# Performance work log

Hardware: AMD Instinct MI355X
Metric: run time of the kernel (lower is better)

## Reference

```python
import jax, jax.numpy as jnp
import numpy as np

B, N, F_IN, F_OUT = 8, 2048, 512, 512


def setup_inputs() -> dict:
    key = jax.random.key(0)
    k1, k2, k3, k4 = jax.random.split(key, 4)
    X = jax.random.normal(k1, (B, N, F_IN), dtype=jnp.float32)
    A = jax.random.uniform(k2, (B, N, N), dtype=jnp.float32)
    # nn.Linear params (kaiming-uniform-ish scale is irrelevant for correctness)
    bound = 1.0 / np.sqrt(F_IN)
    W = jax.random.uniform(k3, (F_IN, F_OUT), dtype=jnp.float32, minval=-bound, maxval=bound)
    b = jax.random.uniform(k4, (F_OUT,), dtype=jnp.float32, minval=-bound, maxval=bound)
    return {"X": X, "A": A, "W": W, "b": b}


def reference(X, A, W, b):
    # A' = A + I  (self-loops)
    A_hat = A + jnp.eye(A.shape[-1], dtype=A.dtype)
    # D^{-1/2}: per-row degree of A'.  torch builds diag_embed + two bmms;
    # mathematically identical to broadcasted row/column scaling.
    d_inv_sqrt = A_hat.sum(axis=-1) ** -0.5                      # [B, N]
    L = A_hat * d_inv_sqrt[:, :, None] * d_inv_sqrt[:, None, :]  # [B, N, N]
    x = X @ W + b                                                # [B, N, F_out]
    return jnp.einsum('bij,bjf->bif', L, x)
```

## Files before the change

### kernel.cpp

```cpp
#include <hip/hip_runtime.h>

#define B_ 8
#define N_ 2048
#define FIN_ 512
#define FOUT_ 512

typedef __attribute__((ext_vector_type(8))) short short8;
typedef __attribute__((ext_vector_type(4))) float floatx4;
typedef __attribute__((ext_vector_type(4))) unsigned short ushortx4;
typedef __attribute__((ext_vector_type(8))) unsigned short ushortx8;

__device__ inline unsigned short f2bf(float f) {
    union { float f; unsigned int u; } x; x.f = f;
    unsigned int r = x.u + 0x7FFFu + ((x.u >> 16) & 1u);
    return (unsigned short)(r >> 16);
}

__device__ inline void glds16(const void* g, void* l) {
    __builtin_amdgcn_global_load_lds(
        (const __attribute__((address_space(1))) void*)g,
        (__attribute__((address_space(3))) void*)l, 16, 0, 0);
}

__global__ __launch_bounds__(256) void degree_cast_kernel(
    const float* __restrict__ A, float* __restrict__ dinv,
    unsigned short* __restrict__ Abf) {
    int row = blockIdx.x;
    size_t base = (size_t)row * N_;
    const float4* A4 = (const float4*)(A + base);
    int t = threadIdx.x;
    float4 v0 = A4[t];
    float4 v1 = A4[t + 256];
    ushortx4 p0, p1;
    p0[0] = f2bf(v0.x); p0[1] = f2bf(v0.y); p0[2] = f2bf(v0.z); p0[3] = f2bf(v0.w);
    p1[0] = f2bf(v1.x); p1[1] = f2bf(v1.y); p1[2] = f2bf(v1.z); p1[3] = f2bf(v1.w);
    *(ushortx4*)(Abf + base + t * 4) = p0;
    *(ushortx4*)(Abf + base + (t + 256) * 4) = p1;
    float s = v0.x + v0.y + v0.z + v0.w + v1.x + v1.y + v1.z + v1.w;
#pragma unroll
    for (int off = 32; off > 0; off >>= 1) s += __shfl_down(s, off, 64);
    __shared__ float red[4];
    if ((t & 63) == 0) red[t >> 6] = s;
    __syncthreads();
    if (t == 0) dinv[row] = rsqrtf(red[0] + red[1] + red[2] + red[3] + 1.0f);
}

__global__ __launch_bounds__(256) void castX_kernel(const float* __restrict__ X,
                                                    unsigned short* __restrict__ Xbf) {
    size_t e0 = ((size_t)blockIdx.x * 256 + threadIdx.x) * 8;
    float4 a0 = *(const float4*)(X + e0);
    float4 a1 = *(const float4*)(X + e0 + 4);
    float av[8] = {a0.x, a0.y, a0.z, a0.w, a1.x, a1.y, a1.z, a1.w};
    ushortx8 p;
#pragma unroll
    for (int r = 0; r < 8; ++r) p[r] = f2bf(av[r]);
    *(ushortx8*)(Xbf + e0) = p;
}

__global__ __launch_bounds__(256) void transposeW_kernel(const float* __restrict__ W,
                                                         unsigned short* __restrict__ Wt) {
    __shared__ float tile[32][33];
    int bx = blockIdx.x * 32;
    int by = blockIdx.y * 32;
    int tx = threadIdx.x, ty = threadIdx.y;
#pragma unroll
    for (int r = 0; r < 32; r += 8)
        tile[ty + r][tx] = W[(size_t)(by + ty + r) * FOUT_ + bx + tx];
    __syncthreads();
#pragma unroll
    for (int r = 0; r < 32; r += 8)
        Wt[(size_t)(bx + ty + r) * FIN_ + by + tx] = f2bf(tile[tx][ty + r]);
}


__global__ __launch_bounds__(256) void gemm1_kernel(
    const unsigned short* __restrict__ Abase,
    const unsigned short* __restrict__ Btbase,
    unsigned short* __restrict__ XwT,
    const float* __restrict__ bias,
    const float* __restrict__ dinv) {
    __shared__ __align__(16) char smem[65536];

    int t = threadIdx.x;
    int lane = t & 63;
    int wave = t >> 6;
    int wr = wave >> 1, wc = wave & 1;
    int q = lane >> 4, m = lane & 15;
    int n0 = blockIdx.x * 128;
    int m0 = blockIdx.y * 128;

    int srow = t >> 3;
    int scol = (((t & 7) ^ (srow & 7)) * 8);
    int x0 = ((q ^ (m & 7)) * 16);
    int x1 = x0 ^ 64;

    floatx4 acc[4][4];
#pragma unroll
    for (int mi = 0; mi < 4; ++mi)
#pragma unroll
        for (int ni = 0; ni < 4; ++ni)
            acc[mi][ni] = (floatx4){0.f, 0.f, 0.f, 0.f};

    const unsigned short* gA = Abase + (size_t)(m0 + srow) * FIN_ + scol;
    const unsigned short* gB = Btbase + (size_t)(n0 + srow) * FIN_ + scol;

#define STAGE1(bufi) do {                                              \
        char* lA = smem + (bufi) * 32768 + wave * 1024;                \
        char* lB = smem + (bufi) * 32768 + 16384 + wave * 1024;        \
        _Pragma("unroll")                                              \
        for (int u = 0; u < 4; ++u) {                                  \
            glds16(gA + (size_t)(u * 32) * FIN_, lA + u * 4096);       \
            glds16(gB + (size_t)(u * 32) * FIN_, lB + u * 4096);       \
        }                                                              \
        gA += 64; gB += 64;                                            \
    } while (0)

    STAGE1(0);
    STAGE1(1);

    const int NT = FIN_ / 64;
    for (int kt = 0; kt < NT; ++kt) {
        if (kt < NT - 1) asm volatile("s_waitcnt vmcnt(8)" ::: "memory");
        else             asm volatile("s_waitcnt vmcnt(0)" ::: "memory");
        __builtin_amdgcn_sched_barrier(0);
        __builtin_amdgcn_s_barrier();
        const char* As = smem + (kt & 1) * 32768;
        const char* Bs = As + 16384;
        short8 af0[4], bf0[4], af1[4], bf1[4];
#pragma unroll
        for (int mi = 0; mi < 4; ++mi)
            af0[mi] = *(const short8*)(As + (wr * 64 + mi * 16 + m) * 128 + x0);
#pragma unroll
        for (int ni = 0; ni < 4; ++ni)
            bf0[ni] = *(const short8*)(Bs + (wc * 64 + ni * 16 + m) * 128 + x0);
#pragma unroll
        for (int mi = 0; mi < 4; ++mi)
            af1[mi] = *(const short8*)(As + (wr * 64 + mi * 16 + m) * 128 + x1);
#pragma unroll
        for (int ni = 0; ni < 4; ++ni)
            bf1[ni] = *(const short8*)(Bs + (wc * 64 + ni * 16 + m) * 128 + x1);
        asm volatile("s_waitcnt lgkmcnt(8)" ::: "memory");
        __builtin_amdgcn_sched_barrier(0);
        __builtin_amdgcn_s_setprio(1);
#pragma unroll
        for (int mi = 0; mi < 4; ++mi)
#pragma unroll
            for (int ni = 0; ni < 4; ++ni)
                acc[mi][ni] = __builtin_amdgcn_mfma_f32_16x16x32_bf16(
                    af0[mi], bf0[ni], acc[mi][ni], 0, 0, 0);
        __builtin_amdgcn_s_setprio(0);
        asm volatile("s_waitcnt lgkmcnt(0)" ::: "memory");
        __builtin_amdgcn_sched_barrier(0);
        __builtin_amdgcn_s_barrier();
        if (kt + 2 < NT) STAGE1(kt & 1);
        __builtin_amdgcn_sched_barrier(0);
        __builtin_amdgcn_s_setprio(1);
#pragma unroll
        for (int mi = 0; mi < 4; ++mi)
#pragma unroll
            for (int ni = 0; ni < 4; ++ni)
                acc[mi][ni] = __builtin_amdgcn_mfma_f32_16x16x32_bf16(
                    af1[mi], bf1[ni], acc[mi][ni], 0, 0, 0);
        __builtin_amdgcn_s_setprio(0);
    }
#undef STAGE1

    unsigned short* T = (unsigned short*)smem;
#pragma unroll
    for (int mi = 0; mi < 4; ++mi) {
        int row = wr * 64 + mi * 16 + q * 4;
        float4 dv = *(const float4*)(dinv + m0 + row);
        float dr[4] = {dv.x, dv.y, dv.z, dv.w};
#pragma unroll
        for (int ni = 0; ni < 4; ++ni) {
            int col = wc * 64 + ni * 16 + m;
            float bv = bias[n0 + col];
            ushortx4 pk;
#pragma unroll
            for (int r = 0; r < 4; ++r) pk[r] = f2bf((acc[mi][ni][r] + bv) * dr[r]);
            *(ushortx4*)(T + col * 136 + row) = pk;
        }
    }
    __syncthreads();
    int f  = t >> 1;
    int c0 = (t & 1) * 64;
    int bb = m0 >> 11;
    int node0 = (m0 & 2047) + c0;
    unsigned short* dst = XwT + ((size_t)bb * FOUT_ + n0 + f) * N_ + node0;
    const unsigned short* src = T + f * 136 + c0;
#pragma unroll
    for (int u = 0; u < 8; ++u)
        *(ushortx8*)(dst + u * 8) = *(const ushortx8*)(src + u * 8);
}

__global__ __launch_bounds__(128) void gemm2_kernel(
    const unsigned short* __restrict__ Abf,
    const unsigned short* __restrict__ XwT,
    const float* __restrict__ dinv,
    float* __restrict__ out) {
    __shared__ __align__(16) char smem[24576];
    char* As = smem;
    char* Bs = smem + 8192;

    int t = threadIdx.x;
    int lane = t & 63;
    int wave = t >> 6;
    int q = lane >> 4, m = lane & 15;

    int id = blockIdx.x;
    int b  = id & 7;
    int s  = id >> 3;
    int n0 = (s & 3) * 128;
    int m0 = (s >> 2) * 64;

    const unsigned short* Ab = Abf + (size_t)b * N_ * N_;
    const unsigned short* Bb = XwT + (size_t)b * FOUT_ * N_;

    int srow = t >> 3;
    int scol = (((t & 7) ^ (srow & 7)) * 8);
    int x0 = ((q ^ (m & 7)) * 16);
    int x1 = x0 ^ 64;

    floatx4 acc[4][4];
#pragma unroll
    for (int mi = 0; mi < 4; ++mi)
#pragma unroll
        for (int ni = 0; ni < 4; ++ni)
            acc[mi][ni] = (floatx4){0.f, 0.f, 0.f, 0.f};

    const unsigned short* gA = Ab + (size_t)(m0 + srow) * N_ + scol;
    const unsigned short* gB = Bb + (size_t)(n0 + srow) * N_ + scol;
    char* lA = As + wave * 1024;
    char* lB = Bs + wave * 1024;

    for (int kt = 0; kt < N_ / 64; ++kt) {
#pragma unroll
        for (int u = 0; u < 4; ++u)
            glds16(gA + (size_t)(u * 16) * N_, lA + u * 2048);
#pragma unroll
        for (int u = 0; u < 8; ++u)
            glds16(gB + (size_t)(u * 16) * N_, lB + u * 2048);
        gA += 64; gB += 64;
        __syncthreads();

#pragma unroll
        for (int sl = 0; sl < 2; ++sl) {
            int xs = sl ? x1 : x0;
            short8 af[4], bfr[4];
#pragma unroll
            for (int mi = 0; mi < 4; ++mi)
                af[mi] = *(const short8*)(As + (mi * 16 + m) * 128 + xs);
#pragma unroll
            for (int ni = 0; ni < 4; ++ni)
                bfr[ni] = *(const short8*)(Bs + (wave * 64 + ni * 16 + m) * 128 + xs);
#pragma unroll
            for (int mi = 0; mi < 4; ++mi)
#pragma unroll
                for (int ni = 0; ni < 4; ++ni)
                    acc[mi][ni] = __builtin_amdgcn_mfma_f32_16x16x32_bf16(
                        af[mi], bfr[ni], acc[mi][ni], 0, 0, 0);
        }
        __syncthreads();
    }

    float* C = out + (size_t)b * N_ * FOUT_;
#pragma unroll
    for (int mi = 0; mi < 4; ++mi) {
        int rowb = m0 + mi * 16 + q * 4;
        float4 dv = *(const float4*)(dinv + b * N_ + rowb);
        float dr[4] = {dv.x, dv.y, dv.z, dv.w};
#pragma unroll
        for (int ni = 0; ni < 4; ++ni) {
            int col = n0 + wave * 64 + ni * 16 + m;
            ushortx4 yv = *(const ushortx4*)(Bb + (size_t)col * N_ + rowb);
#pragma unroll
            for (int r = 0; r < 4; ++r) {
                union { unsigned int u; float f; } yc; yc.u = ((unsigned int)yv[r]) << 16;
                C[(size_t)(rowb + r) * FOUT_ + col] = dr[r] * (acc[mi][ni][r] + yc.f);
            }
        }
    }
}

extern "C" void kernel_launch(void* const* d_in, const int* in_sizes, int n_in,
                              void* d_out, int out_size, void* d_ws, size_t ws_size,
                              hipStream_t stream) {
    const float* X    = (const float*)d_in[0];
    const float* A    = (const float*)d_in[1];
    const float* W    = (const float*)d_in[2];
    const float* bias = (const float*)d_in[3];
    float* out = (float*)d_out;
    char* ws = (char*)d_ws;

    float* dinv          = (float*)(ws);
    unsigned short* Xbf  = (unsigned short*)(ws + (1u << 16));
    unsigned short* Wt   = (unsigned short*)(ws + (1u << 16) + 16777216u);
    unsigned short* XwT  = (unsigned short*)(ws + (1u << 16) + 16777216u + 524288u);
    unsigned short* Abf  = (unsigned short*)(ws + (1u << 16) + 16777216u + 524288u + 16777216u);

    degree_cast_kernel<<<B_ * N_, 256, 0, stream>>>(A, dinv, Abf);
    castX_kernel<<<((size_t)B_ * N_ * FIN_) / 2048, 256, 0, stream>>>(X, Xbf);
    transposeW_kernel<<<dim3(FOUT_ / 32, FIN_ / 32), dim3(32, 8), 0, stream>>>(W, Wt);

    gemm1_kernel<<<dim3(FOUT_ / 128, (B_ * N_) / 128), 256, 0, stream>>>(
        Xbf, Wt, XwT, bias, dinv);

    gemm2_kernel<<<1024, 128, 0, stream>>>(Abf, XwT, dinv, out);
}
```

Baseline: 297.2 us.

## Split-K gemm2 with 128x128 tiles and atomic accumulation, seed output in gemm1

```diff
diff --git a/kernel.cpp b/kernel.cpp
--- a/kernel.cpp
+++ b/kernel.cpp
@@ -78,7 +78,8 @@
     const unsigned short* __restrict__ Btbase,
     unsigned short* __restrict__ XwT,
     const float* __restrict__ bias,
-    const float* __restrict__ dinv) {
+    const float* __restrict__ dinv,
+    float* __restrict__ out) {
     __shared__ __align__(16) char smem[65536];
 
     int t = threadIdx.x;
@@ -177,7 +178,11 @@
             float bv = bias[n0 + col];
             ushortx4 pk;
 #pragma unroll
-            for (int r = 0; r < 4; ++r) pk[r] = f2bf((acc[mi][ni][r] + bv) * dr[r]);
+            for (int r = 0; r < 4; ++r) {
+                float fv = (acc[mi][ni][r] + bv) * dr[r];
+                pk[r] = f2bf(fv);
+                out[(size_t)(m0 + row + r) * FOUT_ + (n0 + col)] = dr[r] * fv;
+            }
             *(ushortx4*)(T + col * 136 + row) = pk;
         }
     }
@@ -193,25 +198,27 @@
         *(ushortx8*)(dst + u * 8) = *(const ushortx8*)(src + u * 8);
 }
 
-__global__ __launch_bounds__(128) void gemm2_kernel(
+__global__ __launch_bounds__(256, 3) void gemm2_kernel(
     const unsigned short* __restrict__ Abf,
     const unsigned short* __restrict__ XwT,
     const float* __restrict__ dinv,
     float* __restrict__ out) {
-    __shared__ __align__(16) char smem[24576];
+    __shared__ __align__(16) char smem[32768];
     char* As = smem;
-    char* Bs = smem + 8192;
+    char* Bs = smem + 16384;
 
     int t = threadIdx.x;
     int lane = t & 63;
     int wave = t >> 6;
+    int wr = wave >> 1, wc = wave & 1;
     int q = lane >> 4, m = lane & 15;
 
     int id = blockIdx.x;
     int b  = id & 7;
-    int s  = id >> 3;
+    int s  = (id >> 3) & 63;
+    int kh = id >> 9;
     int n0 = (s & 3) * 128;
-    int m0 = (s >> 2) * 64;
+    int m0 = (s >> 2) * 128;
 
     const unsigned short* Ab = Abf + (size_t)b * N_ * N_;
     const unsigned short* Bb = XwT + (size_t)b * FOUT_ * N_;
@@ -228,18 +235,17 @@
         for (int ni = 0; ni < 4; ++ni)
             acc[mi][ni] = (floatx4){0.f, 0.f, 0.f, 0.f};
 
-    const unsigned short* gA = Ab + (size_t)(m0 + srow) * N_ + scol;
-    const unsigned short* gB = Bb + (size_t)(n0 + srow) * N_ + scol;
+    const unsigned short* gA = Ab + (size_t)(m0 + srow) * N_ + kh * 1024 + scol;
+    const unsigned short* gB = Bb + (size_t)(n0 + srow) * N_ + kh * 1024 + scol;
     char* lA = As + wave * 1024;
     char* lB = Bs + wave * 1024;
 
-    for (int kt = 0; kt < N_ / 64; ++kt) {
-#pragma unroll
-        for (int u = 0; u < 4; ++u)
-            glds16(gA + (size_t)(u * 16) * N_, lA + u * 2048);
-#pragma unroll
-        for (int u = 0; u < 8; ++u)
-            glds16(gB + (size_t)(u * 16) * N_, lB + u * 2048);
+    for (int kt = 0; kt < 16; ++kt) {
+#pragma unroll
+        for (int u = 0; u < 4; ++u) {
+            glds16(gA + (size_t)(u * 32) * N_, lA + u * 4096);
+            glds16(gB + (size_t)(u * 32) * N_, lB + u * 4096);
+        }
         gA += 64; gB += 64;
         __syncthreads();
 
@@ -249,10 +255,10 @@
             short8 af[4], bfr[4];
 #pragma unroll
             for (int mi = 0; mi < 4; ++mi)
-                af[mi] = *(const short8*)(As + (mi * 16 + m) * 128 + xs);
+                af[mi] = *(const short8*)(As + (wr * 64 + mi * 16 + m) * 128 + xs);
 #pragma unroll
             for (int ni = 0; ni < 4; ++ni)
-                bfr[ni] = *(const short8*)(Bs + (wave * 64 + ni * 16 + m) * 128 + xs);
+                bfr[ni] = *(const short8*)(Bs + (wc * 64 + ni * 16 + m) * 128 + xs);
 #pragma unroll
             for (int mi = 0; mi < 4; ++mi)
 #pragma unroll
@@ -266,18 +272,16 @@
     float* C = out + (size_t)b * N_ * FOUT_;
 #pragma unroll
     for (int mi = 0; mi < 4; ++mi) {
-        int rowb = m0 + mi * 16 + q * 4;
+        int rowb = m0 + wr * 64 + mi * 16 + q * 4;
         float4 dv = *(const float4*)(dinv + b * N_ + rowb);
         float dr[4] = {dv.x, dv.y, dv.z, dv.w};
 #pragma unroll
         for (int ni = 0; ni < 4; ++ni) {
-            int col = n0 + wave * 64 + ni * 16 + m;
-            ushortx4 yv = *(const ushortx4*)(Bb + (size_t)col * N_ + rowb);
-#pragma unroll
-            for (int r = 0; r < 4; ++r) {
-                union { unsigned int u; float f; } yc; yc.u = ((unsigned int)yv[r]) << 16;
-                C[(size_t)(rowb + r) * FOUT_ + col] = dr[r] * (acc[mi][ni][r] + yc.f);
-            }
+            int col = n0 + wc * 64 + ni * 16 + m;
+#pragma unroll
+            for (int r = 0; r < 4; ++r)
+                unsafeAtomicAdd(&C[(size_t)(rowb + r) * FOUT_ + col],
+                                dr[r] * acc[mi][ni][r]);
         }
     }
 }
@@ -303,7 +307,7 @@
     transposeW_kernel<<<dim3(FOUT_ / 32, FIN_ / 32), dim3(32, 8), 0, stream>>>(W, Wt);
 
     gemm1_kernel<<<dim3(FOUT_ / 128, (B_ * N_) / 128), 256, 0, stream>>>(
-        Xbf, Wt, XwT, bias, dinv);
-
-    gemm2_kernel<<<1024, 128, 0, stream>>>(Abf, XwT, dinv, out);
-}
+        Xbf, Wt, XwT, bias, dinv, out);
+
+    gemm2_kernel<<<1024, 256, 0, stream>>>(Abf, XwT, dinv, out);
+}
```

New measurement: 343.7 us. +15.7%, slower.
